# Kernel optimization log

Measured on AMD Instinct MI355X. Metric: run time of the kernel, lower is better.

Reference implementation:

```python
import jax, jax.numpy as jnp
import numpy as np

B, S, D_IN, D_HID, D_OUT, PE_DIM = 8, 4096, 1024, 1024, 1024, 16


def sinusoidal_embeddings(batch_size, seq_len, dim):
    positions = jnp.arange(seq_len)[:, None].astype(jnp.float32)
    div_term = jnp.exp(jnp.arange(0, dim, 2).astype(jnp.float32) * (-jnp.log(10000.0) / dim))
    pe = jnp.zeros((seq_len, dim), dtype=jnp.float32)
    pe = pe.at[:, 0::2].set(jnp.sin(positions * div_term))
    pe = pe.at[:, 1::2].set(jnp.cos(positions * div_term))
    return jnp.broadcast_to(pe, (batch_size, seq_len, dim))


def setup_inputs() -> dict:
    key = jax.random.key(0)
    ks = jax.random.split(key, 8)
    d_cat = D_IN + PE_DIM
    # a_logit drawn so that sigmoid(a_logit) lands in the stable decay range [0.9, 0.999]
    u = jax.random.uniform(ks[1], (D_HID,), minval=0.9, maxval=0.999)
    a_logit = jnp.log(u) - jnp.log1p(-u)  # logit
    scale_in = 1.0 / np.sqrt(d_cat)
    scale_h = 1.0 / np.sqrt(D_HID)
    return {
        "x": jax.random.normal(ks[0], (B, S, D_IN), dtype=jnp.float32),
        "a_logit": a_logit.astype(jnp.float32),
        "W_dx": jax.random.normal(ks[2], (d_cat, D_OUT), dtype=jnp.float32) * scale_in,
        "b_dx": jnp.zeros((D_OUT,), dtype=jnp.float32),
        "W_in": jax.random.normal(ks[3], (d_cat, D_HID), dtype=jnp.float32) * scale_in,
        "b_in": jnp.zeros((D_HID,), dtype=jnp.float32),
        "W_out": jax.random.normal(ks[4], (D_HID, D_OUT), dtype=jnp.float32) * scale_h,
        "b_out": jnp.zeros((D_OUT,), dtype=jnp.float32),
    }


def reference(x, a_logit, W_dx, b_dx, W_in, b_in, W_out, b_out):
    batch, seq, _ = x.shape
    a = jax.nn.sigmoid(a_logit)  # (d_hidden,)
    # rnn_pos_embedding: concat 16-dim sinusoidal PE
    xc = jnp.concatenate([x, sinusoidal_embeddings(batch, seq, PE_DIM)], axis=-1)
    dx = xc @ W_dx + b_dx  # (B, S, d_out)
    u = xc @ W_in + b_in  # (B, S, d_hidden)
    # rnn_norm_input
    u = jnp.sqrt(1.0 - a ** 2) * u
    u = jnp.transpose(u, (1, 0, 2))  # (S, B, d_hidden)

    def step(h, xt):
        h = a * h + xt
        return h, h

    init = jnp.zeros((batch, a.shape[0]), dtype=x.dtype)
    _, h = jax.lax.scan(step, init, u)
    h = jnp.transpose(h, (1, 0, 2))  # (B, S, d_hidden)
    return (dx + h @ W_out + b_out) / 2
```

## Files before the change

### kernel.cpp

```cpp
#include <hip/hip_runtime.h>
#include <hip/hip_bf16.h>
#include <math.h>

#define B_DIM 8
#define S_DIM 4096
#define DIN   1024
#define DHID  1024
#define DOUT  1024
#define LDA   1024
#define MTOT  (B_DIM*S_DIM)
#define NCHUNK 32
#define LCHUNK 128

typedef __attribute__((ext_vector_type(8))) short bf16x8;
typedef __attribute__((ext_vector_type(4))) float f32x4;
typedef __attribute__((ext_vector_type(4))) unsigned short u16x4;
typedef __attribute__((ext_vector_type(8))) unsigned short u16x8;

__device__ __forceinline__ unsigned short f2bf(float f) {
  union { float f; unsigned u; } v; v.f = f;
  unsigned r = v.u + 0x7fffu + ((v.u >> 16) & 1u);
  return (unsigned short)(r >> 16);
}
__device__ __forceinline__ float bf2f(unsigned short h) {
  union { unsigned u; float f; } v; v.u = ((unsigned)h) << 16;
  return v.f;
}

#define GLOAD16(g, l)                                                         \
  __builtin_amdgcn_global_load_lds(                                           \
      (const __attribute__((address_space(1))) void*)(g),                     \
      (__attribute__((address_space(3))) void*)(l), 16, 0, 0)

#define BAR()   __builtin_amdgcn_s_barrier()
#define LGKM0() do { asm volatile("s_waitcnt lgkmcnt(0)" ::: "memory");       \
                     __builtin_amdgcn_sched_barrier(0); } while (0)


__global__ void prep_a_kernel(const float* __restrict__ logit,
                              float* __restrict__ avec, float* __restrict__ svec) {
  int d = blockIdx.x * 256 + threadIdx.x;
  if (d >= DHID) return;
  float a = 1.f / (1.f + expf(-logit[d]));
  avec[d] = a;
  svec[d] = sqrtf(fmaxf(0.f, 1.f - a * a));
}

__global__ __launch_bounds__(256) void transpose_cast_kernel(
    const float* __restrict__ W, unsigned short* __restrict__ Wt) {
  __shared__ float tile[32][33];
  const int N = 1024;
  int kb = blockIdx.x * 32, nb = blockIdx.y * 32;
  int tx = threadIdx.x & 31, ty = threadIdx.x >> 5;
#pragma unroll
  for (int r = 0; r < 32; r += 8)
    tile[ty + r][tx] = W[(size_t)(kb + ty + r) * N + nb + tx];
  __syncthreads();
#pragma unroll
  for (int r = 0; r < 32; r += 8)
    Wt[(size_t)(nb + ty + r) * N + kb + tx] = f2bf(tile[tx][ty + r]);
}

__global__ __launch_bounds__(256) void pew_kernel(const float* __restrict__ W,
                                                  float* __restrict__ PEW) {
  __shared__ float pe[16];
  int t = blockIdx.x;
  if (threadIdx.x < 16) {
    int j = threadIdx.x, i = j >> 1;
    float div = expf(-(float)i * 1.1512925465f);
    float arg = (float)t * div;
    pe[j] = (j & 1) ? cosf(arg) : sinf(arg);
  }
  __syncthreads();
  int col0 = threadIdx.x * 4;
  float a0 = 0.f, a1 = 0.f, a2 = 0.f, a3 = 0.f;
#pragma unroll
  for (int j = 0; j < 16; j++) {
    const float4 wv = *(const float4*)(W + (size_t)(1024 + j) * 1024 + col0);
    float p = pe[j];
    a0 = fmaf(p, wv.x, a0); a1 = fmaf(p, wv.y, a1);
    a2 = fmaf(p, wv.z, a2); a3 = fmaf(p, wv.w, a3);
  }
  float4 o = {a0, a1, a2, a3};
  *(float4*)(PEW + (size_t)t * 1024 + col0) = o;
}

__global__ __launch_bounds__(256) void cast_kernel(const float* __restrict__ x,
                                                   unsigned short* __restrict__ xb) {
  size_t i = ((size_t)blockIdx.x * 256 + threadIdx.x) * 8;
  float4 v0 = *(const float4*)(x + i);
  float4 v1 = *(const float4*)(x + i + 4);
  u16x8 o;
  o[0] = f2bf(v0.x); o[1] = f2bf(v0.y); o[2] = f2bf(v0.z); o[3] = f2bf(v0.w);
  o[4] = f2bf(v1.x); o[5] = f2bf(v1.y); o[6] = f2bf(v1.z); o[7] = f2bf(v1.w);
  *(u16x8*)(xb + i) = o;
}


__device__ __forceinline__ bf16x8 frag(const unsigned short* hb, int row, int slot) {
  int ph = slot ^ (row & 7);
  return *(const bf16x8*)(hb + (size_t)row * 64 + ph * 8);
}

#define READ_A4(dst, base, roff)                                              \
  _Pragma("unroll") for (int mq = 0; mq < 4; mq++)                            \
    _Pragma("unroll") for (int kk = 0; kk < 2; kk++)                          \
      dst[mq][kk] = frag(base, (roff) + mq * 16 + rl, kk * 4 + s);

#define READ_B2(dst, base, roff)                                              \
  _Pragma("unroll") for (int nq = 0; nq < 2; nq++)                            \
    _Pragma("unroll") for (int kk = 0; kk < 2; kk++)                          \
      dst[nq][kk] = frag(base, (roff) + nq * 16 + rl, kk * 4 + s);

#define MFMA_Q(MH, NH, AA, BB)                                                \
  __builtin_amdgcn_s_setprio(1);                                              \
  _Pragma("unroll") for (int mq = 0; mq < 4; mq++)                            \
    _Pragma("unroll") for (int nq = 0; nq < 2; nq++)                          \
      _Pragma("unroll") for (int kk = 0; kk < 2; kk++)                        \
        acc[(MH)*4 + mq][(NH)*2 + nq] =                                       \
            __builtin_amdgcn_mfma_f32_16x16x32_bf16(                          \
                AA[mq][kk], BB[nq][kk], acc[(MH)*4 + mq][(NH)*2 + nq], 0,0,0);\
  __builtin_amdgcn_s_setprio(0);

template <int NSEG>
__device__ __forceinline__ void gemm_pipe4(
    const unsigned short* __restrict__ A0p, const unsigned short* __restrict__ B0p,
    int kt0,
    const unsigned short* __restrict__ A1p, const unsigned short* __restrict__ B1p,
    int kt1,
    int arow0, int bcol0,
    unsigned short (*lA)[2][8192], unsigned short (*lB)[2][8192],
    f32x4 acc[8][4]) {
  const int tid = threadIdx.x;
  const int lane = tid & 63, w = tid >> 6;
  const int wrow = w >> 2, wcol = w & 3;
  const int rl = lane & 15, s = lane >> 4;
  const int br = (wcol & 1) * 64;
  const int kt = (NSEG == 2) ? (kt0 + kt1) : kt0;

  const int c1 = tid, c2 = tid + 512;
  const int r1 = c1 >> 3, sl1 = (c1 & 7) ^ (r1 & 7);
  const int r2 = c2 >> 3, sl2 = (c2 & 7) ^ (r2 & 7);
  const unsigned short* gAa0 = A0p + (size_t)(arow0 + r1) * LDA + sl1 * 8;
  const unsigned short* gAb0 = A0p + (size_t)(arow0 + r2) * LDA + sl2 * 8;
  const unsigned short* gBa0 = B0p + (size_t)(bcol0 + r1) * LDA + sl1 * 8;
  const unsigned short* gBb0 = B0p + (size_t)(bcol0 + r2) * LDA + sl2 * 8;
  const unsigned short* gAa1 = gAa0; const unsigned short* gAb1 = gAb0;
  const unsigned short* gBa1 = gBa0; const unsigned short* gBb1 = gBb0;
  if (NSEG == 2) {
    gAa1 = A1p + (size_t)(arow0 + r1) * LDA + sl1 * 8;
    gAb1 = A1p + (size_t)(arow0 + r2) * LDA + sl2 * 8;
    gBa1 = B1p + (size_t)(bcol0 + r1) * LDA + sl1 * 8;
    gBb1 = B1p + (size_t)(bcol0 + r2) * LDA + sl2 * 8;
  }
  const size_t hstep = (size_t)128 * LDA;

  auto stg_a = [&](int tt, int h) {
    const unsigned short* pa = gAa0; const unsigned short* pb = gAb0; int rel = tt;
    if (NSEG == 2 && tt >= kt0) { pa = gAa1; pb = gAb1; rel = tt - kt0; }
    size_t o = (size_t)rel * 64 + (size_t)h * hstep;
    GLOAD16(pa + o, &lA[tt & 1][h][(size_t)c1 * 8]);
    GLOAD16(pb + o, &lA[tt & 1][h][(size_t)c2 * 8]);
  };
  auto stg_b = [&](int tt, int h) {
    const unsigned short* pa = gBa0; const unsigned short* pb = gBb0; int rel = tt;
    if (NSEG == 2 && tt >= kt0) { pa = gBa1; pb = gBb1; rel = tt - kt0; }
    size_t o = (size_t)rel * 64 + (size_t)h * hstep;
    GLOAD16(pa + o, &lB[tt & 1][h][(size_t)c1 * 8]);
    GLOAD16(pb + o, &lB[tt & 1][h][(size_t)c2 * 8]);
  };

  stg_a(0, 0); stg_a(0, 1); stg_b(0, 0); stg_b(0, 1);
  stg_b(1, 0); stg_b(1, 1);
  asm volatile("s_waitcnt vmcnt(4)" ::: "memory");
  BAR();
  __builtin_amdgcn_sched_barrier(0);

  for (int t = 0; t < kt; ++t) {
    const unsigned short* Ac = &lA[t & 1][wrow][0];
    const unsigned short* Bc = &lB[t & 1][wcol >> 1][0];
    bf16x8 alo[4][2], ahi[4][2], blo[2][2], bhi[2][2];

    READ_A4(alo, Ac, 0);
    READ_B2(blo, Bc, br);
    if (t + 1 < kt) stg_a(t + 1, 0);
    BAR(); LGKM0();
    MFMA_Q(0, 0, alo, blo);
    BAR();

    READ_B2(bhi, Bc, br + 32);
    if (t + 1 < kt) stg_a(t + 1, 1);
    BAR(); LGKM0();
    MFMA_Q(0, 1, alo, bhi);
    BAR();

    READ_A4(ahi, Ac, 64);
    if (t + 2 < kt) stg_b(t + 2, 0);
    BAR(); LGKM0();
    MFMA_Q(1, 1, ahi, bhi);
    BAR();

    if (t + 2 < kt) {
      stg_b(t + 2, 1);
      asm volatile("s_waitcnt vmcnt(4)" ::: "memory");
    } else {
      asm volatile("s_waitcnt vmcnt(0)" ::: "memory");
    }
    BAR();
    __builtin_amdgcn_sched_barrier(0);
    MFMA_Q(1, 0, ahi, blo);
  }
}

__global__ __launch_bounds__(512, 2) void gemm_u_kernel(
    const unsigned short* __restrict__ xb, const unsigned short* __restrict__ Wtin,
    const float* __restrict__ b_in, const float* __restrict__ svec,
    const float* __restrict__ PEWin, unsigned short* __restrict__ u) {
  __shared__ __align__(16) unsigned short lA[2][2][8192];
  __shared__ __align__(16) unsigned short lB[2][2][8192];
  f32x4 acc[8][4];
  const f32x4 z = {0.f, 0.f, 0.f, 0.f};
#pragma unroll
  for (int i = 0; i < 8; i++)
#pragma unroll
    for (int n = 0; n < 4; n++) acc[i][n] = z;

  int bid = blockIdx.x;
  int swz = (bid & 7) * 64 + (bid >> 3);
  int bcol = swz >> 7, brow = swz & 127;

  gemm_pipe4<1>(xb, Wtin, LDA / 64, xb, Wtin, 0, brow * 256, bcol * 256, lA, lB, acc);

  const int lane = threadIdx.x & 63, w = threadIdx.x >> 6;
  const int wrow = w >> 2, wcol = w & 3;
  const int rl = lane & 15, s = lane >> 4;
  const int colb = bcol * 256 + wcol * 64 + rl;
  const int rowb = brow * 256 + wrow * 128 + s * 4;
#pragma unroll
  for (int n = 0; n < 4; n++) {
    int col = colb + n * 16;
    float bi = b_in[col], sv = svec[col];
#pragma unroll
    for (int i = 0; i < 8; i++) {
#pragma unroll
      for (int r = 0; r < 4; r++) {
        int row = rowb + i * 16 + r;
        float peb = PEWin[(size_t)((row & (S_DIM - 1)) << 10) + col];
        u[(size_t)row * DHID + col] = f2bf((acc[i][n][r] + bi + peb) * sv);
      }
    }
  }
}

__global__ __launch_bounds__(512, 2) void gemm_out_kernel(
    const unsigned short* __restrict__ xb, const unsigned short* __restrict__ Wtdx,
    const unsigned short* __restrict__ h, const unsigned short* __restrict__ Wtout,
    const float* __restrict__ b_dx, const float* __restrict__ b_out,
    const float* __restrict__ PEWdx, float* __restrict__ out) {
  __shared__ __align__(16) unsigned short lA[2][2][8192];
  __shared__ __align__(16) unsigned short lB[2][2][8192];
  f32x4 acc[8][4];
  const f32x4 z = {0.f, 0.f, 0.f, 0.f};
#pragma unroll
  for (int i = 0; i < 8; i++)
#pragma unroll
    for (int n = 0; n < 4; n++) acc[i][n] = z;

  int bid = blockIdx.x;
  int swz = (bid & 7) * 64 + (bid >> 3);
  int bcol = swz >> 7, brow = swz & 127;

  gemm_pipe4<2>(xb, Wtdx, LDA / 64, h, Wtout, LDA / 64, brow * 256, bcol * 256,
                lA, lB, acc);

  const int lane = threadIdx.x & 63, w = threadIdx.x >> 6;
  const int wrow = w >> 2, wcol = w & 3;
  const int rl = lane & 15, s = lane >> 4;
  const int colb = bcol * 256 + wcol * 64 + rl;
  const int rowb = brow * 256 + wrow * 128 + s * 4;
#pragma unroll
  for (int n = 0; n < 4; n++) {
    int col = colb + n * 16;
    float bb = b_dx[col] + b_out[col];
#pragma unroll
    for (int i = 0; i < 8; i++) {
#pragma unroll
      for (int r = 0; r < 4; r++) {
        int row = rowb + i * 16 + r;
        float peb = PEWdx[(size_t)((row & (S_DIM - 1)) << 10) + col];
        out[(size_t)row * DOUT + col] = 0.5f * (acc[i][n][r] + bb + peb);
      }
    }
  }
}


__global__ __launch_bounds__(256) void scan1_kernel(
    const float* __restrict__ avec, unsigned short* __restrict__ uh,
    float* __restrict__ carry) {
  int b = blockIdx.x >> 5, c = blockIdx.x & 31;
  int d0 = threadIdx.x * 4;
  float4 a4 = *(const float4*)(avec + d0);
  unsigned short* p = uh + ((size_t)(b * S_DIM + c * LCHUNK)) * DHID + d0;
  float h0 = 0.f, h1 = 0.f, h2 = 0.f, h3 = 0.f;
#pragma unroll 4
  for (int t = 0; t < LCHUNK; t++) {
    u16x4 v = *(u16x4*)(p + (size_t)t * DHID);
    h0 = fmaf(a4.x, h0, bf2f(v.x));
    h1 = fmaf(a4.y, h1, bf2f(v.y));
    h2 = fmaf(a4.z, h2, bf2f(v.z));
    h3 = fmaf(a4.w, h3, bf2f(v.w));
    v.x = f2bf(h0); v.y = f2bf(h1); v.z = f2bf(h2); v.w = f2bf(h3);
    *(u16x4*)(p + (size_t)t * DHID) = v;
  }
  float4 cv = {h0, h1, h2, h3};
  *(float4*)(carry + ((size_t)b * NCHUNK + c) * DHID + d0) = cv;
}

__global__ __launch_bounds__(256) void scan2_kernel(
    const float* __restrict__ avec, const float* __restrict__ carry,
    float* __restrict__ Hprev) {
  int gid = blockIdx.x * 256 + threadIdx.x;
  int b = gid >> 10, d = gid & 1023;
  float a = avec[d];
  float aL = a;
#pragma unroll
  for (int i = 0; i < 7; i++) aL *= aL;
  float H = 0.f;
#pragma unroll
  for (int c = 0; c < NCHUNK; c++) {
    size_t idx = ((size_t)b * NCHUNK + c) * DHID + d;
    Hprev[idx] = H;
    H = aL * H + carry[idx];
  }
}

__global__ __launch_bounds__(256) void scan3_kernel(
    const float* __restrict__ avec, unsigned short* __restrict__ uh,
    const float* __restrict__ Hprev) {
  int b = blockIdx.x >> 5, c = blockIdx.x & 31;
  int d0 = threadIdx.x * 4;
  float4 Hp = *(const float4*)(Hprev + ((size_t)b * NCHUNK + c) * DHID + d0);
  if (Hp.x == 0.f && Hp.y == 0.f && Hp.z == 0.f && Hp.w == 0.f) return;
  float4 a4 = *(const float4*)(avec + d0);
  float p0 = a4.x * Hp.x, p1 = a4.y * Hp.y, p2 = a4.z * Hp.z, p3 = a4.w * Hp.w;
  unsigned short* p = uh + ((size_t)(b * S_DIM + c * LCHUNK)) * DHID + d0;
#pragma unroll 4
  for (int t = 0; t < LCHUNK; t++) {
    u16x4 v = *(u16x4*)(p + (size_t)t * DHID);
    v.x = f2bf(bf2f(v.x) + p0);
    v.y = f2bf(bf2f(v.y) + p1);
    v.z = f2bf(bf2f(v.z) + p2);
    v.w = f2bf(bf2f(v.w) + p3);
    *(u16x4*)(p + (size_t)t * DHID) = v;
    p0 *= a4.x; p1 *= a4.y; p2 *= a4.z; p3 *= a4.w;
  }
}


extern "C" void kernel_launch(void* const* d_in, const int* in_sizes, int n_in,
                              void* d_out, int out_size, void* d_ws, size_t ws_size,
                              hipStream_t stream) {
  const float* x       = (const float*)d_in[0];
  const float* a_logit = (const float*)d_in[1];
  const float* W_dx    = (const float*)d_in[2];
  const float* b_dx    = (const float*)d_in[3];
  const float* W_in    = (const float*)d_in[4];
  const float* b_in    = (const float*)d_in[5];
  const float* W_out   = (const float*)d_in[6];
  const float* b_out   = (const float*)d_in[7];
  float* out = (float*)d_out;

  char* ws = (char*)d_ws;
  size_t off = 0;
  auto alloc = [&](size_t bytes) {
    void* p = ws + off;
    off += (bytes + 255) & ~(size_t)255;
    return p;
  };
  unsigned short* xb    = (unsigned short*)alloc((size_t)MTOT * 1024 * 2);
  unsigned short* Wtdx  = (unsigned short*)alloc((size_t)1024 * 1024 * 2);
  unsigned short* Wtin  = (unsigned short*)alloc((size_t)1024 * 1024 * 2);
  unsigned short* Wtout = (unsigned short*)alloc((size_t)1024 * 1024 * 2);
  unsigned short* uh    = (unsigned short*)alloc((size_t)MTOT * 1024 * 2);
  float* PEWdx = (float*)alloc((size_t)S_DIM * 1024 * 4);
  float* PEWin = (float*)alloc((size_t)S_DIM * 1024 * 4);
  float* carry = (float*)alloc((size_t)B_DIM * NCHUNK * DHID * 4);
  float* Hprev = (float*)alloc((size_t)B_DIM * NCHUNK * DHID * 4);
  float* avec  = (float*)alloc(DHID * 4);
  float* svec  = (float*)alloc(DHID * 4);
  (void)ws_size; (void)in_sizes; (void)n_in; (void)out_size;

  prep_a_kernel<<<4, 256, 0, stream>>>(a_logit, avec, svec);
  transpose_cast_kernel<<<dim3(32, 32), 256, 0, stream>>>(W_dx, Wtdx);
  transpose_cast_kernel<<<dim3(32, 32), 256, 0, stream>>>(W_in, Wtin);
  transpose_cast_kernel<<<dim3(32, 32), 256, 0, stream>>>(W_out, Wtout);
  pew_kernel<<<S_DIM, 256, 0, stream>>>(W_dx, PEWdx);
  pew_kernel<<<S_DIM, 256, 0, stream>>>(W_in, PEWin);
  cast_kernel<<<MTOT * 1024 / 8 / 256, 256, 0, stream>>>(x, xb);

  gemm_u_kernel<<<512, 512, 0, stream>>>(xb, Wtin, b_in, svec, PEWin, uh);

  scan1_kernel<<<B_DIM * NCHUNK, 256, 0, stream>>>(avec, uh, carry);
  scan2_kernel<<<32, 256, 0, stream>>>(avec, carry, Hprev);
  scan3_kernel<<<B_DIM * NCHUNK, 256, 0, stream>>>(avec, uh, Hprev);

  gemm_out_kernel<<<512, 512, 0, stream>>>(xb, Wtdx, uh, Wtout, b_dx, b_out,
                                           PEWdx, out);
}
```

Before: 412.8 us.

## Restructure GEMM pipelines and fold biases into positional-embedding tables

```diff
diff --git a/kernel.cpp b/kernel.cpp
--- a/kernel.cpp
+++ b/kernel.cpp
@@ -33,6 +33,7 @@
       (__attribute__((address_space(3))) void*)(l), 16, 0, 0)
 
 #define BAR()   __builtin_amdgcn_s_barrier()
+#define SCHED0() __builtin_amdgcn_sched_barrier(0)
 #define LGKM0() do { asm volatile("s_waitcnt lgkmcnt(0)" ::: "memory");       \
                      __builtin_amdgcn_sched_barrier(0); } while (0)
 
@@ -62,7 +63,10 @@
 }
 
 __global__ __launch_bounds__(256) void pew_kernel(const float* __restrict__ W,
-                                                  float* __restrict__ PEW) {
+                                                  const float* __restrict__ ba,
+                                                  const float* __restrict__ bb,
+                                                  float sb,
+                                                  float* __restrict__ PEB) {
   __shared__ float pe[16];
   int t = blockIdx.x;
   if (threadIdx.x < 16) {
@@ -73,7 +77,10 @@
   }
   __syncthreads();
   int col0 = threadIdx.x * 4;
-  float a0 = 0.f, a1 = 0.f, a2 = 0.f, a3 = 0.f;
+  float4 bav = *(const float4*)(ba + col0);
+  float4 bbv = *(const float4*)(bb + col0);
+  float a0 = bav.x + sb * bbv.x, a1 = bav.y + sb * bbv.y;
+  float a2 = bav.z + sb * bbv.z, a3 = bav.w + sb * bbv.w;
 #pragma unroll
   for (int j = 0; j < 16; j++) {
     const float4 wv = *(const float4*)(W + (size_t)(1024 + j) * 1024 + col0);
@@ -82,7 +89,7 @@
     a2 = fmaf(p, wv.z, a2); a3 = fmaf(p, wv.w, a3);
   }
   float4 o = {a0, a1, a2, a3};
-  *(float4*)(PEW + (size_t)t * 1024 + col0) = o;
+  *(float4*)(PEB + (size_t)t * 1024 + col0) = o;
 }
 
 __global__ __launch_bounds__(256) void cast_kernel(const float* __restrict__ x,
@@ -97,7 +104,7 @@
 }
 
 
-__device__ __forceinline__ bf16x8 frag(const unsigned short* hb, int row, int slot) {
+__device__ __forceinline__ bf16x8 frag64(const unsigned short* hb, int row, int slot) {
   int ph = slot ^ (row & 7);
   return *(const bf16x8*)(hb + (size_t)row * 64 + ph * 8);
 }
@@ -105,117 +112,96 @@
 #define READ_A4(dst, base, roff)                                              \
   _Pragma("unroll") for (int mq = 0; mq < 4; mq++)                            \
     _Pragma("unroll") for (int kk = 0; kk < 2; kk++)                          \
-      dst[mq][kk] = frag(base, (roff) + mq * 16 + rl, kk * 4 + s);
+      dst[mq][kk] = frag64(base, (roff) + mq * 16 + rl, kk * 4 + s);
 
 #define READ_B2(dst, base, roff)                                              \
   _Pragma("unroll") for (int nq = 0; nq < 2; nq++)                            \
     _Pragma("unroll") for (int kk = 0; kk < 2; kk++)                          \
-      dst[nq][kk] = frag(base, (roff) + nq * 16 + rl, kk * 4 + s);
-
-#define MFMA_Q(MH, NH, AA, BB)                                                \
+      dst[nq][kk] = frag64(base, (roff) + nq * 16 + rl, kk * 4 + s);
+
+#define MFMA_Q(MH, NH, BB)                                                    \
   __builtin_amdgcn_s_setprio(1);                                              \
   _Pragma("unroll") for (int mq = 0; mq < 4; mq++)                            \
     _Pragma("unroll") for (int nq = 0; nq < 2; nq++)                          \
       _Pragma("unroll") for (int kk = 0; kk < 2; kk++)                        \
         acc[(MH)*4 + mq][(NH)*2 + nq] =                                       \
             __builtin_amdgcn_mfma_f32_16x16x32_bf16(                          \
-                AA[mq][kk], BB[nq][kk], acc[(MH)*4 + mq][(NH)*2 + nq], 0,0,0);\
+                a[mq][kk], BB[nq][kk], acc[(MH)*4 + mq][(NH)*2 + nq], 0,0,0); \
   __builtin_amdgcn_s_setprio(0);
 
-template <int NSEG>
-__device__ __forceinline__ void gemm_pipe4(
-    const unsigned short* __restrict__ A0p, const unsigned short* __restrict__ B0p,
-    int kt0,
-    const unsigned short* __restrict__ A1p, const unsigned short* __restrict__ B1p,
-    int kt1,
-    int arow0, int bcol0,
+__device__ __forceinline__ void gemm_pipe2(
+    const unsigned short* __restrict__ A,
+    const unsigned short* __restrict__ Bt,
+    int kt, int arow0, int brow0,
     unsigned short (*lA)[2][8192], unsigned short (*lB)[2][8192],
     f32x4 acc[8][4]) {
   const int tid = threadIdx.x;
   const int lane = tid & 63, w = tid >> 6;
   const int wrow = w >> 2, wcol = w & 3;
   const int rl = lane & 15, s = lane >> 4;
-  const int br = (wcol & 1) * 64;
-  const int kt = (NSEG == 2) ? (kt0 + kt1) : kt0;
 
   const int c1 = tid, c2 = tid + 512;
   const int r1 = c1 >> 3, sl1 = (c1 & 7) ^ (r1 & 7);
   const int r2 = c2 >> 3, sl2 = (c2 & 7) ^ (r2 & 7);
-  const unsigned short* gAa0 = A0p + (size_t)(arow0 + r1) * LDA + sl1 * 8;
-  const unsigned short* gAb0 = A0p + (size_t)(arow0 + r2) * LDA + sl2 * 8;
-  const unsigned short* gBa0 = B0p + (size_t)(bcol0 + r1) * LDA + sl1 * 8;
-  const unsigned short* gBb0 = B0p + (size_t)(bcol0 + r2) * LDA + sl2 * 8;
-  const unsigned short* gAa1 = gAa0; const unsigned short* gAb1 = gAb0;
-  const unsigned short* gBa1 = gBa0; const unsigned short* gBb1 = gBb0;
-  if (NSEG == 2) {
-    gAa1 = A1p + (size_t)(arow0 + r1) * LDA + sl1 * 8;
-    gAb1 = A1p + (size_t)(arow0 + r2) * LDA + sl2 * 8;
-    gBa1 = B1p + (size_t)(bcol0 + r1) * LDA + sl1 * 8;
-    gBb1 = B1p + (size_t)(bcol0 + r2) * LDA + sl2 * 8;
-  }
+  const unsigned short* pA1 = A + (size_t)(arow0 + r1) * LDA + sl1 * 8;
+  const unsigned short* pA2 = A + (size_t)(arow0 + r2) * LDA + sl2 * 8;
+  const unsigned short* pB1 = Bt + (size_t)(brow0 + r1) * LDA + sl1 * 8;
+  const unsigned short* pB2 = Bt + (size_t)(brow0 + r2) * LDA + sl2 * 8;
   const size_t hstep = (size_t)128 * LDA;
 
-  auto stg_a = [&](int tt, int h) {
-    const unsigned short* pa = gAa0; const unsigned short* pb = gAb0; int rel = tt;
-    if (NSEG == 2 && tt >= kt0) { pa = gAa1; pb = gAb1; rel = tt - kt0; }
-    size_t o = (size_t)rel * 64 + (size_t)h * hstep;
-    GLOAD16(pa + o, &lA[tt & 1][h][(size_t)c1 * 8]);
-    GLOAD16(pb + o, &lA[tt & 1][h][(size_t)c2 * 8]);
-  };
-  auto stg_b = [&](int tt, int h) {
-    const unsigned short* pa = gBa0; const unsigned short* pb = gBb0; int rel = tt;
-    if (NSEG == 2 && tt >= kt0) { pa = gBa1; pb = gBb1; rel = tt - kt0; }
-    size_t o = (size_t)rel * 64 + (size_t)h * hstep;
-    GLOAD16(pa + o, &lB[tt & 1][h][(size_t)c1 * 8]);
-    GLOAD16(pb + o, &lB[tt & 1][h][(size_t)c2 * 8]);
-  };
-
-  stg_a(0, 0); stg_a(0, 1); stg_b(0, 0); stg_b(0, 1);
-  stg_b(1, 0); stg_b(1, 1);
-  asm volatile("s_waitcnt vmcnt(4)" ::: "memory");
+#define STG_A(t, h) do { size_t _o = (size_t)(t) * 64 + (size_t)(h) * hstep;  \
+    int _b = (t) & 1;                                                         \
+    GLOAD16(pA1 + _o, &lA[_b][h][(size_t)c1 * 8]);                            \
+    GLOAD16(pA2 + _o, &lA[_b][h][(size_t)c2 * 8]); } while (0)
+#define STG_B(t, h) do { size_t _o = (size_t)(t) * 64 + (size_t)(h) * hstep;  \
+    int _b = (t) & 1;                                                         \
+    GLOAD16(pB1 + _o, &lB[_b][h][(size_t)c1 * 8]);                            \
+    GLOAD16(pB2 + _o, &lB[_b][h][(size_t)c2 * 8]); } while (0)
+
+  STG_B(0, 0); STG_B(0, 1); STG_A(0, 0); STG_A(0, 1);
+  STG_B(1, 0); STG_B(1, 1); STG_A(1, 0); STG_A(1, 1);
+  asm volatile("s_waitcnt vmcnt(8)" ::: "memory");
   BAR();
-  __builtin_amdgcn_sched_barrier(0);
-
+
+  const int br = (wcol & 1) * 64;
   for (int t = 0; t < kt; ++t) {
+    const bool st = (t + 2) < kt;
     const unsigned short* Ac = &lA[t & 1][wrow][0];
     const unsigned short* Bc = &lB[t & 1][wcol >> 1][0];
-    bf16x8 alo[4][2], ahi[4][2], blo[2][2], bhi[2][2];
-
-    READ_A4(alo, Ac, 0);
-    READ_B2(blo, Bc, br);
-    if (t + 1 < kt) stg_a(t + 1, 0);
+    bf16x8 a[4][2], b0[2][2], b1[2][2];
+
+    READ_A4(a, Ac, 0);
+    READ_B2(b0, Bc, br);
     BAR(); LGKM0();
-    MFMA_Q(0, 0, alo, blo);
+    MFMA_Q(0, 0, b0);
     BAR();
 
-    READ_B2(bhi, Bc, br + 32);
-    if (t + 1 < kt) stg_a(t + 1, 1);
+    READ_B2(b1, Bc, br + 32);
     BAR(); LGKM0();
-    MFMA_Q(0, 1, alo, bhi);
+    MFMA_Q(0, 1, b1);
     BAR();
 
-    READ_A4(ahi, Ac, 64);
-    if (t + 2 < kt) stg_b(t + 2, 0);
+    READ_A4(a, Ac, 64);
+    if (st) { STG_B(t + 2, 0); STG_B(t + 2, 1); }
     BAR(); LGKM0();
-    MFMA_Q(1, 1, ahi, bhi);
+    MFMA_Q(1, 1, b1);
     BAR();
 
-    if (t + 2 < kt) {
-      stg_b(t + 2, 1);
-      asm volatile("s_waitcnt vmcnt(4)" ::: "memory");
-    } else {
-      asm volatile("s_waitcnt vmcnt(0)" ::: "memory");
-    }
+    if (st) { STG_A(t + 2, 0); STG_A(t + 2, 1); }
     BAR();
-    __builtin_amdgcn_sched_barrier(0);
-    MFMA_Q(1, 0, ahi, blo);
-  }
-}
-
-__global__ __launch_bounds__(512, 2) void gemm_u_kernel(
-    const unsigned short* __restrict__ xb, const unsigned short* __restrict__ Wtin,
-    const float* __restrict__ b_in, const float* __restrict__ svec,
-    const float* __restrict__ PEWin, unsigned short* __restrict__ u) {
+    MFMA_Q(1, 0, b0);
+    if (st) { asm volatile("s_waitcnt vmcnt(8)" ::: "memory"); }
+    else    { asm volatile("s_waitcnt vmcnt(0)" ::: "memory"); }
+    BAR();
+  }
+#undef STG_A
+#undef STG_B
+}
+
+__global__ __launch_bounds__(512, 2) void gemm_out_kernel(
+    const unsigned short* __restrict__ xb, const unsigned short* __restrict__ Wtdx,
+    const unsigned short* __restrict__ h, const unsigned short* __restrict__ Wtout,
+    const float* __restrict__ PEBdx, float* __restrict__ out) {
   __shared__ __align__(16) unsigned short lA[2][2][8192];
   __shared__ __align__(16) unsigned short lB[2][2][8192];
   f32x4 acc[8][4];
@@ -229,7 +215,8 @@
   int swz = (bid & 7) * 64 + (bid >> 3);
   int bcol = swz >> 7, brow = swz & 127;
 
-  gemm_pipe4<1>(xb, Wtin, LDA / 64, xb, Wtin, 0, brow * 256, bcol * 256, lA, lB, acc);
+  gemm_pipe2(xb, Wtdx, LDA / 64, brow * 256, bcol * 256, lA, lB, acc);
+  gemm_pipe2(h, Wtout, LDA / 64, brow * 256, bcol * 256, lA, lB, acc);
 
   const int lane = threadIdx.x & 63, w = threadIdx.x >> 6;
   const int wrow = w >> 2, wcol = w & 3;
@@ -239,56 +226,97 @@
 #pragma unroll
   for (int n = 0; n < 4; n++) {
     int col = colb + n * 16;
-    float bi = b_in[col], sv = svec[col];
 #pragma unroll
     for (int i = 0; i < 8; i++) {
 #pragma unroll
       for (int r = 0; r < 4; r++) {
         int row = rowb + i * 16 + r;
-        float peb = PEWin[(size_t)((row & (S_DIM - 1)) << 10) + col];
-        u[(size_t)row * DHID + col] = f2bf((acc[i][n][r] + bi + peb) * sv);
+        float peb = PEBdx[(size_t)((row & (S_DIM - 1)) << 10) + col];
+        out[(size_t)row * DOUT + col] = 0.5f * (acc[i][n][r] + peb);
       }
     }
   }
 }
 
-__global__ __launch_bounds__(512, 2) void gemm_out_kernel(
-    const unsigned short* __restrict__ xb, const unsigned short* __restrict__ Wtdx,
-    const unsigned short* __restrict__ h, const unsigned short* __restrict__ Wtout,
-    const float* __restrict__ b_dx, const float* __restrict__ b_out,
-    const float* __restrict__ PEWdx, float* __restrict__ out) {
-  __shared__ __align__(16) unsigned short lA[2][2][8192];
-  __shared__ __align__(16) unsigned short lB[2][2][8192];
-  f32x4 acc[8][4];
+
+__device__ __forceinline__ bf16x8 frag32(const unsigned short* hb, int row, int s) {
+  int ph = s ^ ((row >> 1) & 3);
+  return *(const bf16x8*)(hb + (size_t)row * 32 + ph * 8);
+}
+
+__global__ __launch_bounds__(1024) void gemm_u_kernel(
+    const unsigned short* __restrict__ xb, const unsigned short* __restrict__ Wtin,
+    const float* __restrict__ svec, const float* __restrict__ PEBin,
+    unsigned short* __restrict__ u) {
+  __shared__ __align__(16) unsigned short lA[3][8192];
+  __shared__ __align__(16) unsigned short lB[3][8192];
+  f32x4 acc[4][4];
   const f32x4 z = {0.f, 0.f, 0.f, 0.f};
 #pragma unroll
-  for (int i = 0; i < 8; i++)
-#pragma unroll
-    for (int n = 0; n < 4; n++) acc[i][n] = z;
+  for (int m = 0; m < 4; m++)
+#pragma unroll
+    for (int n = 0; n < 4; n++) acc[m][n] = z;
 
   int bid = blockIdx.x;
   int swz = (bid & 7) * 64 + (bid >> 3);
   int bcol = swz >> 7, brow = swz & 127;
 
-  gemm_pipe4<2>(xb, Wtdx, LDA / 64, h, Wtout, LDA / 64, brow * 256, bcol * 256,
-                lA, lB, acc);
-
-  const int lane = threadIdx.x & 63, w = threadIdx.x >> 6;
-  const int wrow = w >> 2, wcol = w & 3;
+  const int tid = threadIdx.x;
+  const int lane = tid & 63, w = tid >> 6;
+  const int wr = w >> 2, wc = w & 3;
   const int rl = lane & 15, s = lane >> 4;
-  const int colb = bcol * 256 + wcol * 64 + rl;
-  const int rowb = brow * 256 + wrow * 128 + s * 4;
+
+  const int r1 = tid >> 2;
+  const int sl1 = (tid & 3) ^ ((r1 >> 1) & 3);
+  const unsigned short* gA = xb   + (size_t)(brow * 256 + r1) * LDA + sl1 * 8;
+  const unsigned short* gB = Wtin + (size_t)(bcol * 256 + r1) * LDA + sl1 * 8;
+
+  const int kt = LDA / 32;
+  auto stage = [&](int t) {
+    int b = t % 3;
+    GLOAD16(gA + (size_t)t * 32, &lA[b][(size_t)tid * 8]);
+    GLOAD16(gB + (size_t)t * 32, &lB[b][(size_t)tid * 8]);
+  };
+
+  stage(0); stage(1);
+  asm volatile("s_waitcnt vmcnt(2)" ::: "memory");
+  BAR(); SCHED0();
+
+  for (int t = 0; t < kt; ++t) {
+    const bool st = (t + 2) < kt;
+    if (st) stage(t + 2);
+    const unsigned short* Ac = lA[t % 3];
+    const unsigned short* Bc = lB[t % 3];
+    bf16x8 af[4], bf[4];
+#pragma unroll
+    for (int m = 0; m < 4; m++) af[m] = frag32(Ac, wr * 64 + m * 16 + rl, s);
+#pragma unroll
+    for (int n = 0; n < 4; n++) bf[n] = frag32(Bc, wc * 64 + n * 16 + rl, s);
+    __builtin_amdgcn_s_setprio(1);
+#pragma unroll
+    for (int m = 0; m < 4; m++)
+#pragma unroll
+      for (int n = 0; n < 4; n++)
+        acc[m][n] = __builtin_amdgcn_mfma_f32_16x16x32_bf16(af[m], bf[n], acc[m][n], 0, 0, 0);
+    __builtin_amdgcn_s_setprio(0);
+    if (st) asm volatile("s_waitcnt vmcnt(2)" ::: "memory");
+    else    asm volatile("s_waitcnt vmcnt(0)" ::: "memory");
+    BAR(); SCHED0();
+  }
+
+  const int colb = bcol * 256 + wc * 64 + rl;
+  const int rowb = brow * 256 + wr * 64 + s * 4;
 #pragma unroll
   for (int n = 0; n < 4; n++) {
     int col = colb + n * 16;
-    float bb = b_dx[col] + b_out[col];
-#pragma unroll
-    for (int i = 0; i < 8; i++) {
+    float sv = svec[col];
+#pragma unroll
+    for (int m = 0; m < 4; m++) {
 #pragma unroll
       for (int r = 0; r < 4; r++) {
-        int row = rowb + i * 16 + r;
-        float peb = PEWdx[(size_t)((row & (S_DIM - 1)) << 10) + col];
-        out[(size_t)row * DOUT + col] = 0.5f * (acc[i][n][r] + bb + peb);
+        int row = rowb + m * 16 + r;
+        float peb = PEBin[(size_t)((row & (S_DIM - 1)) << 10) + col];
+        u[(size_t)row * DHID + col] = f2bf((acc[m][n][r] + peb) * sv);
       }
     }
   }
@@ -383,8 +411,8 @@
   unsigned short* Wtin  = (unsigned short*)alloc((size_t)1024 * 1024 * 2);
   unsigned short* Wtout = (unsigned short*)alloc((size_t)1024 * 1024 * 2);
   unsigned short* uh    = (unsigned short*)alloc((size_t)MTOT * 1024 * 2);
-  float* PEWdx = (float*)alloc((size_t)S_DIM * 1024 * 4);
-  float* PEWin = (float*)alloc((size_t)S_DIM * 1024 * 4);
+  float* PEBdx = (float*)alloc((size_t)S_DIM * 1024 * 4);
+  float* PEBin = (float*)alloc((size_t)S_DIM * 1024 * 4);
   float* carry = (float*)alloc((size_t)B_DIM * NCHUNK * DHID * 4);
   float* Hprev = (float*)alloc((size_t)B_DIM * NCHUNK * DHID * 4);
   float* avec  = (float*)alloc(DHID * 4);
@@ -395,16 +423,15 @@
   transpose_cast_kernel<<<dim3(32, 32), 256, 0, stream>>>(W_dx, Wtdx);
   transpose_cast_kernel<<<dim3(32, 32), 256, 0, stream>>>(W_in, Wtin);
   transpose_cast_kernel<<<dim3(32, 32), 256, 0, stream>>>(W_out, Wtout);
-  pew_kernel<<<S_DIM, 256, 0, stream>>>(W_dx, PEWdx);
-  pew_kernel<<<S_DIM, 256, 0, stream>>>(W_in, PEWin);
+  pew_kernel<<<S_DIM, 256, 0, stream>>>(W_dx, b_dx, b_out, 1.0f, PEBdx);
+  pew_kernel<<<S_DIM, 256, 0, stream>>>(W_in, b_in, b_in, 0.0f, PEBin);
   cast_kernel<<<MTOT * 1024 / 8 / 256, 256, 0, stream>>>(x, xb);
 
-  gemm_u_kernel<<<512, 512, 0, stream>>>(xb, Wtin, b_in, svec, PEWin, uh);
+  gemm_u_kernel<<<512, 1024, 0, stream>>>(xb, Wtin, svec, PEBin, uh);
 
   scan1_kernel<<<B_DIM * NCHUNK, 256, 0, stream>>>(avec, uh, carry);
   scan2_kernel<<<32, 256, 0, stream>>>(avec, carry, Hprev);
   scan3_kernel<<<B_DIM * NCHUNK, 256, 0, stream>>>(avec, uh, Hprev);
 
-  gemm_out_kernel<<<512, 512, 0, stream>>>(xb, Wtdx, uh, Wtout, b_dx, b_out,
-                                           PEWdx, out);
-}
+  gemm_out_kernel<<<512, 512, 0, stream>>>(xb, Wtdx, uh, Wtout, PEBdx, out);
+}
```

Result: no change. 418.9 us (+1.5%).
